# Optimization experiments

Measured on AMD Instinct MI355X. Metric: run time of the kernel, lower is better.

## Reference

```python
import jax, jax.numpy as jnp
import numpy as np

B, S, D_IN, D_OUT, H = 4, 2048, 1024, 1024, 16
D_HEAD = D_OUT // H


def setup_inputs() -> dict:
    key = jax.random.key(0)
    ks = jax.random.split(key, 6)
    sc = 0.02
    return {
        "x": jax.random.normal(ks[0], (B, S, D_IN), dtype=jnp.float32),
        "Wq": jax.random.normal(ks[1], (D_IN, D_OUT), dtype=jnp.float32) * sc,
        "Wk": jax.random.normal(ks[2], (D_IN, D_OUT), dtype=jnp.float32) * sc,
        "Wv": jax.random.normal(ks[3], (D_IN, D_OUT), dtype=jnp.float32) * sc,
        "Wo": jax.random.normal(ks[4], (D_OUT, D_OUT), dtype=jnp.float32) * sc,
        "bo": jnp.zeros((D_OUT,), dtype=jnp.float32),
    }


def reference(x, Wq, Wk, Wv, Wo, bo):
    n_batch, n_tok, _ = x.shape
    # QKV projections (no bias), reshape to [B, H, S, Dh]
    q = (x @ Wq).reshape(n_batch, n_tok, H, D_HEAD).transpose(0, 2, 1, 3)
    k = (x @ Wk).reshape(n_batch, n_tok, H, D_HEAD).transpose(0, 2, 1, 3)
    v = (x @ Wv).reshape(n_batch, n_tok, H, D_HEAD).transpose(0, 2, 1, 3)
    # scores [B, H, S, S], causal mask, scaled softmax
    scores = jnp.einsum('bhqd,bhkd->bhqk', q, k)
    causal = jnp.tril(jnp.ones((n_tok, n_tok), dtype=bool))
    scores = jnp.where(causal, scores, -jnp.inf)
    attn = jax.nn.softmax(scores / jnp.sqrt(jnp.float32(D_HEAD)), axis=-1)
    # dropout in eval mode -> identity
    ctx = jnp.einsum('bhqk,bhkd->bhqd', attn, v)
    ctx = ctx.transpose(0, 2, 1, 3).reshape(n_batch, n_tok, D_OUT)
    return ctx @ Wo + bo
```

## Files before the change

### kernel.cpp

```cpp
#include <hip/hip_runtime.h>


#define S_LEN 2048
#define DMODEL 1024
#define NB 4

typedef unsigned short u16;
typedef float f32x4 __attribute__((ext_vector_type(4)));
typedef short s16x8 __attribute__((ext_vector_type(8)));
typedef __bf16 bf16x8 __attribute__((ext_vector_type(8)));

__device__ __forceinline__ u16 f2bf(float f) {
  return __builtin_bit_cast(u16, (__bf16)f);
}

__device__ __forceinline__ f32x4 mfma16(s16x8 a, s16x8 b, f32x4 c) {
  return __builtin_amdgcn_mfma_f32_16x16x32_bf16(
      __builtin_bit_cast(bf16x8, a), __builtin_bit_cast(bf16x8, b), c, 0, 0, 0);
}

__device__ __forceinline__ void gload_lds16(void* lds, const void* g) {
  __builtin_amdgcn_global_load_lds(
      (const __attribute__((address_space(1))) void*)g,
      (__attribute__((address_space(3))) void*)lds, 16, 0, 0);
}

__device__ __forceinline__ s16x8 lds_frag(const u16* lds, int row, int colb) {
  int addr = (row << 7) + (colb ^ ((row & 7) << 4));
  return *(const s16x8*)((const char*)lds + addr);
}

struct G8 {
  u16 As[3][256 * 64];
  u16 Bs[3][128 * 64];
};

template <int NT>
__device__ __forceinline__ void gemm8ph(const u16* __restrict__ A,
                                        const u16* __restrict__ Bt,
                                        int m0, int n0, G8& L,
                                        f32x4 (&acc)[4][4], int tid) {
  constexpr int K = NT * 64;
  const int lane = tid & 63;
  const int wr = (tid >> 6) >> 1, wc = (tid >> 6) & 1;

  auto SA = [&](int buf, int kt) {
    const u16* g = A + (size_t)m0 * K + kt * 64;
    #pragma unroll
    for (int it = 0; it < 4; ++it) {
      int o = (tid + it * 512) << 4;
      int r = o >> 7, c = o & 127;
      gload_lds16((char*)L.As[buf] + o,
                  (const char*)(g + (size_t)r * K) + (c ^ ((r & 7) << 4)));
    }
  };
  auto SB = [&](int buf, int kt) {
    const u16* g = Bt + (size_t)n0 * K + kt * 64;
    #pragma unroll
    for (int it = 0; it < 2; ++it) {
      int o = (tid + it * 512) << 4;
      int r = o >> 7, c = o & 127;
      gload_lds16((char*)L.Bs[buf] + o,
                  (const char*)(g + (size_t)r * K) + (c ^ ((r & 7) << 4)));
    }
  };

  SA(0, 0); SB(0, 0);
  SA(1, 1); SB(1, 1);
  asm volatile("s_waitcnt vmcnt(6)" ::: "memory");
  asm volatile("s_barrier" ::: "memory");

  int cb = 0;
  for (int t = 0; t < NT; ++t) {
    const u16* Ac = L.As[cb];
    const u16* Bc = L.Bs[cb];
    int nxt = cb + 2; if (nxt >= 3) nxt -= 3;
    bool pf = (t + 2 < NT);
    #pragma unroll
    for (int ph = 0; ph < 2; ++ph) {
      s16x8 a[4], b[4];
      #pragma unroll
      for (int f = 0; f < 4; ++f) {
        a[f] = lds_frag(Ac, wr * 64 + f * 16 + (lane & 15), ph * 64 + ((lane >> 4) << 4));
        b[f] = lds_frag(Bc, wc * 64 + f * 16 + (lane & 15), ph * 64 + ((lane >> 4) << 4));
      }
      if (pf) { if (ph == 0) SA(nxt, t + 2); else SB(nxt, t + 2); }
      asm volatile("s_barrier" ::: "memory");
      asm volatile("s_waitcnt lgkmcnt(0)" ::: "memory");
      __builtin_amdgcn_sched_barrier(0);
      __builtin_amdgcn_s_setprio(1);
      #pragma unroll
      for (int mf = 0; mf < 4; ++mf)
        #pragma unroll
        for (int nf = 0; nf < 4; ++nf)
          acc[mf][nf] = mfma16(a[mf], b[nf], acc[mf][nf]);
      __builtin_amdgcn_s_setprio(0);
    }
    if (pf) asm volatile("s_waitcnt vmcnt(6)" ::: "memory");
    else    asm volatile("s_waitcnt vmcnt(0)" ::: "memory");
    asm volatile("s_barrier" ::: "memory");
    cb = (cb + 1 == 3) ? 0 : cb + 1;
  }
}

__global__ __launch_bounds__(256) void castx_kernel(const float4* __restrict__ x,
                                                    ushort4* __restrict__ xb) {
  int i = blockIdx.x * 256 + threadIdx.x;
  float4 v = x[i];
  ushort4 o;
  o.x = f2bf(v.x); o.y = f2bf(v.y); o.z = f2bf(v.z); o.w = f2bf(v.w);
  xb[i] = o;
}

__global__ __launch_bounds__(256) void wtrans_kernel(
    const float* __restrict__ W0, const float* __restrict__ W1,
    const float* __restrict__ W2, const float* __restrict__ W3,
    u16* __restrict__ T0, u16* __restrict__ T1, u16* __restrict__ T2, u16* __restrict__ T3) {
  int z = blockIdx.z;
  const float* W = (z == 0) ? W0 : (z == 1) ? W1 : (z == 2) ? W2 : W3;
  u16* T = (z == 0) ? T0 : (z == 1) ? T1 : (z == 2) ? T2 : T3;
  __shared__ float t[32][33];
  int n0 = blockIdx.x << 5, k0 = blockIdx.y << 5;
  int tx = threadIdx.x & 31, ty = threadIdx.x >> 5;
  #pragma unroll
  for (int j = 0; j < 4; ++j)
    t[ty + (j << 3)][tx] = W[(size_t)(k0 + ty + (j << 3)) * DMODEL + n0 + tx];
  __syncthreads();
  #pragma unroll
  for (int j = 0; j < 4; ++j)
    T[(size_t)(n0 + ty + (j << 3)) * DMODEL + k0 + tx] = f2bf(t[tx][ty + (j << 3)]);
}

__global__ __launch_bounds__(512, 2) void qkv8_kernel(
    const u16* __restrict__ xb, const u16* __restrict__ WqkvT,
    u16* __restrict__ Qo, u16* __restrict__ Ko, u16* __restrict__ Vo) {
  __shared__ G8 L;
  int bid = blockIdx.x;
  int f = (bid & 7) * 96 + (bid >> 3);
  int m0 = (f / 24) << 8, n0 = (f % 24) << 7;
  int tid = threadIdx.x, lane = tid & 63;
  int wr = (tid >> 6) >> 1, wc = (tid >> 6) & 1;
  f32x4 acc[4][4] = {};
  gemm8ph<16>(xb, WqkvT, m0, n0, L, acc, tid);
  #pragma unroll
  for (int mf = 0; mf < 4; ++mf)
    #pragma unroll
    for (int nf = 0; nf < 4; ++nf)
      #pragma unroll
      for (int i = 0; i < 4; ++i) {
        int rm = m0 + wr * 64 + mf * 16 + ((lane >> 4) << 2) + i;
        int cn = n0 + wc * 64 + nf * 16 + (lane & 15);
        int bb = rm >> 11, s = rm & (S_LEN - 1);
        int z = cn >> 10, c1 = cn & 1023;
        int h = c1 >> 6, d = c1 & 63;
        u16* out = (z == 0) ? Qo : (z == 1) ? Ko : Vo;
        float v = acc[mf][nf][i] * ((z == 0) ? 0.18033688f : 1.0f);
        out[((size_t)((bb << 4) + h) << 17) + ((size_t)s << 6) + d] = f2bf(v);
      }
}

__global__ __launch_bounds__(256) void vtrans_kernel(const u16* __restrict__ V,
                                                     u16* __restrict__ Vt) {
  __shared__ u16 t[64][72];
  int s0 = blockIdx.x << 6;
  size_t bh = blockIdx.y;
  const u16* Vb = V + (bh << 17);
  u16* Vtb = Vt + (bh << 17);
  int tid = threadIdx.x;
  #pragma unroll
  for (int it = 0; it < 2; ++it) {
    int o = (tid + (it << 8)) << 3;
    int r = o >> 6, c = o & 63;
    const ushort4* p = (const ushort4*)(Vb + (((size_t)(s0 + r)) << 6) + c);
    ushort4 v0 = p[0], v1 = p[1];
    t[r][c + 0] = v0.x; t[r][c + 1] = v0.y; t[r][c + 2] = v0.z; t[r][c + 3] = v0.w;
    t[r][c + 4] = v1.x; t[r][c + 5] = v1.y; t[r][c + 6] = v1.z; t[r][c + 7] = v1.w;
  }
  __syncthreads();
  #pragma unroll
  for (int it = 0; it < 2; ++it) {
    int o = (tid + (it << 8)) << 3;
    int d = o >> 6, sl = o & 63;
    ushort4 a, b;
    a.x = t[sl + 0][d]; a.y = t[sl + 1][d]; a.z = t[sl + 2][d]; a.w = t[sl + 3][d];
    b.x = t[sl + 4][d]; b.y = t[sl + 5][d]; b.z = t[sl + 6][d]; b.w = t[sl + 7][d];
    ushort4* q = (ushort4*)(Vtb + ((size_t)d << 11) + s0 + sl);
    q[0] = a; q[1] = b;
  }
}

__global__ __launch_bounds__(512, 4) void attn_kernel(const u16* __restrict__ Q,
                                                      const u16* __restrict__ K,
                                                      const u16* __restrict__ Vt,
                                                      u16* __restrict__ ctx) {
  __shared__ u16 Ks[2][64 * 64];
  __shared__ u16 Vts[2][64 * 64];
  __shared__ u16 Ps[8][16 * 64];
  int bh = blockIdx.x, pid = blockIdx.y;
  int tid = threadIdx.x, lane = tid & 63, w = tid >> 6;
  const u16* Qb = Q + ((size_t)bh << 17);
  const u16* Kb = K + ((size_t)bh << 17);
  const u16* Vtb = Vt + ((size_t)bh << 17);
  int bb = bh >> 4, h = bh & 15;
  u16* Pw = Ps[w];

  s16x8 onesf;
  #pragma unroll
  for (int j = 0; j < 8; ++j) onesf[j] = (short)0x3F80;

  auto stage = [&](int buf, int k0) {
    int o = tid << 4;
    int r = o >> 7, c = o & 127;
    int csrc = c ^ ((r & 7) << 4);
    gload_lds16((char*)Ks[buf] + o, (const char*)(Kb + ((size_t)(k0 + r) << 6)) + csrc);
    gload_lds16((char*)Vts[buf] + o, (const char*)(Vtb + ((size_t)r << 11) + k0) + csrc);
  };

  for (int ph = 0; ph < 2; ++ph) {
    int qblk = ph ? (15 - pid) : pid;
    int q0 = qblk << 7;
    int qw = q0 + (w << 4);

    s16x8 qf[2];
    #pragma unroll
    for (int ks = 0; ks < 2; ++ks) {
      int row = qw + (lane & 15);
      int col = ks * 32 + ((lane >> 4) << 3);
      qf[ks] = *(const s16x8*)(Qb + ((size_t)row << 6) + col);
    }

    f32x4 acc_o[4] = {};
    f32x4 acc_l = {};

    int ntiles = (q0 >> 6) + 2;
    int cur = 0;
    stage(0, 0);
    __syncthreads();
    for (int t = 0; t < ntiles; ++t) {
      int k0 = t << 6;
      if (t + 1 < ntiles) stage(cur ^ 1, (t + 1) << 6);

      bool active = (k0 <= qw + 15);
      if (active) {
        const u16* Kc = Ks[cur];
        const u16* Vc = Vts[cur];
        f32x4 sc[4] = {};
        #pragma unroll
        for (int ks = 0; ks < 2; ++ks) {
          s16x8 kf[4];
          #pragma unroll
          for (int nf = 0; nf < 4; ++nf)
            kf[nf] = lds_frag(Kc, nf * 16 + (lane & 15), ks * 64 + ((lane >> 4) << 4));
          __builtin_amdgcn_s_setprio(1);
          #pragma unroll
          for (int nf = 0; nf < 4; ++nf)
            sc[nf] = mfma16(qf[ks], kf[nf], sc[nf]);
          __builtin_amdgcn_s_setprio(0);
        }

        bool need_mask = (k0 + 63) > qw;
        if (need_mask) {
          #pragma unroll
          for (int i = 0; i < 4; ++i) {
            int q = qw + ((lane >> 4) << 2) + i;
            #pragma unroll
            for (int nf = 0; nf < 4; ++nf) {
              int kv = k0 + nf * 16 + (lane & 15);
              sc[nf][i] = (kv <= q) ? sc[nf][i] : -3.0e38f;
            }
          }
        }
        #pragma unroll
        for (int nf = 0; nf < 4; ++nf)
          #pragma unroll
          for (int i = 0; i < 4; ++i)
            sc[nf][i] = __builtin_amdgcn_exp2f(sc[nf][i]);

        #pragma unroll
        for (int nf = 0; nf < 4; ++nf)
          #pragma unroll
          for (int i = 0; i < 4; ++i) {
            int r = ((lane >> 4) << 2) + i;
            int cb = (nf * 16 + (lane & 15)) << 1;
            *(u16*)((char*)Pw + (r << 7) + (cb ^ ((r & 7) << 4))) = f2bf(sc[nf][i]);
          }
        asm volatile("s_waitcnt lgkmcnt(0)" ::: "memory");
        __builtin_amdgcn_sched_barrier(0);

        #pragma unroll
        for (int ks = 0; ks < 2; ++ks) {
          s16x8 pf = lds_frag(Pw, lane & 15, ks * 64 + ((lane >> 4) << 4));
          s16x8 vf[4];
          #pragma unroll
          for (int nf = 0; nf < 4; ++nf)
            vf[nf] = lds_frag(Vc, nf * 16 + (lane & 15), ks * 64 + ((lane >> 4) << 4));
          __builtin_amdgcn_s_setprio(1);
          #pragma unroll
          for (int nf = 0; nf < 4; ++nf)
            acc_o[nf] = mfma16(pf, vf[nf], acc_o[nf]);
          acc_l = mfma16(pf, onesf, acc_l);
          __builtin_amdgcn_s_setprio(0);
        }
      }
      __syncthreads();
      cur ^= 1;
    }

    #pragma unroll
    for (int i = 0; i < 4; ++i) acc_l[i] = 1.0f / acc_l[i];
    #pragma unroll
    for (int nf = 0; nf < 4; ++nf)
      #pragma unroll
      for (int i = 0; i < 4; ++i) {
        int q = qw + ((lane >> 4) << 2) + i;
        int d = nf * 16 + (lane & 15);
        float v = acc_o[nf][i] * acc_l[i];
        ctx[(((size_t)(bb << 11) + q) << 10) + (h << 6) + d] = f2bf(v);
      }
  }
}

__global__ __launch_bounds__(512, 2) void out8_kernel(const u16* __restrict__ ctx,
                                                      const u16* __restrict__ WoT,
                                                      const float* __restrict__ bo,
                                                      float* __restrict__ out) {
  __shared__ G8 L;
  int bid = blockIdx.x;
  int f = (bid & 7) * 32 + (bid >> 3);
  int m0 = (f >> 3) << 8, n0 = (f & 7) << 7;
  int tid = threadIdx.x, lane = tid & 63;
  int wr = (tid >> 6) >> 1, wc = (tid >> 6) & 1;
  f32x4 acc[4][4] = {};
  gemm8ph<16>(ctx, WoT, m0, n0, L, acc, tid);
  #pragma unroll
  for (int mf = 0; mf < 4; ++mf)
    #pragma unroll
    for (int nf = 0; nf < 4; ++nf)
      #pragma unroll
      for (int i = 0; i < 4; ++i) {
        int rm = m0 + wr * 64 + mf * 16 + ((lane >> 4) << 2) + i;
        int cn = n0 + wc * 64 + nf * 16 + (lane & 15);
        out[(size_t)rm * DMODEL + cn] = acc[mf][nf][i] + bo[cn];
      }
}

extern "C" void kernel_launch(void* const* d_in, const int* in_sizes, int n_in,
                              void* d_out, int out_size, void* d_ws, size_t ws_size,
                              hipStream_t stream) {
  const float* x  = (const float*)d_in[0];
  const float* Wq = (const float*)d_in[1];
  const float* Wk = (const float*)d_in[2];
  const float* Wv = (const float*)d_in[3];
  const float* Wo = (const float*)d_in[4];
  const float* bo = (const float*)d_in[5];
  float* out = (float*)d_out;

  char* ws = (char*)d_ws;
  const size_t SZ_T = (size_t)NB * S_LEN * DMODEL * 2;
  const size_t SZ_W = (size_t)DMODEL * DMODEL * 2;
  u16* xb  = (u16*)(ws);
  u16* WqT = (u16*)(ws + SZ_T);
  u16* WkT = (u16*)(ws + SZ_T + 1 * SZ_W);
  u16* WvT = (u16*)(ws + SZ_T + 2 * SZ_W);
  u16* WoT = (u16*)(ws + SZ_T + 3 * SZ_W);
  u16* Qb  = (u16*)(ws + 1 * SZ_T + 4 * SZ_W);
  u16* Kb  = (u16*)(ws + 2 * SZ_T + 4 * SZ_W);
  u16* Vb  = (u16*)(ws + 3 * SZ_T + 4 * SZ_W);
  u16* Vtb = (u16*)(ws + 4 * SZ_T + 4 * SZ_W);
  u16* ctx = xb;

  castx_kernel<<<dim3((NB * S_LEN * DMODEL / 4) / 256), dim3(256), 0, stream>>>(
      (const float4*)x, (ushort4*)xb);
  wtrans_kernel<<<dim3(32, 32, 4), dim3(256), 0, stream>>>(Wq, Wk, Wv, Wo,
                                                           WqT, WkT, WvT, WoT);
  qkv8_kernel<<<dim3(768), dim3(512), 0, stream>>>(xb, WqT, Qb, Kb, Vb);
  vtrans_kernel<<<dim3(32, 64), dim3(256), 0, stream>>>(Vb, Vtb);
  attn_kernel<<<dim3(64, 8), dim3(512), 0, stream>>>(Qb, Kb, Vtb, ctx);
  out8_kernel<<<dim3(256), dim3(512), 0, stream>>>(ctx, WoT, bo, out);
}
```

Measured before the change: 160.0 us.

## Restructure attention to 32x32 MFMA with transposed scores and register-resident P

The attention kernel moves from 16x16x32 to 32x32x16 MFMA tiles and computes S transposed (K·Q), so each lane owns one query row. P is converted to bf16 in registers and rearranged with v_permlane32_swap instead of going through LDS. Each warp now covers 32 query rows, with 4 warps per block instead of 8. The row sum becomes a per-lane scalar accumulation instead of an MFMA against a ones vector. This removes the LDS round trip, its waitcnt barrier and the extra MFMA for l, but raises register pressure and halves the threads per block.

```diff
diff --git a/kernel.cpp b/kernel.cpp
--- a/kernel.cpp
+++ b/kernel.cpp
@@ -6,7 +6,10 @@
 #define NB 4
 
 typedef unsigned short u16;
+typedef unsigned int u32;
 typedef float f32x4 __attribute__((ext_vector_type(4)));
+typedef float f32x16 __attribute__((ext_vector_type(16)));
+typedef int i32x4 __attribute__((ext_vector_type(4)));
 typedef short s16x8 __attribute__((ext_vector_type(8)));
 typedef __bf16 bf16x8 __attribute__((ext_vector_type(8)));
 
@@ -17,6 +20,17 @@
 __device__ __forceinline__ f32x4 mfma16(s16x8 a, s16x8 b, f32x4 c) {
   return __builtin_amdgcn_mfma_f32_16x16x32_bf16(
       __builtin_bit_cast(bf16x8, a), __builtin_bit_cast(bf16x8, b), c, 0, 0, 0);
+}
+
+__device__ __forceinline__ f32x16 mfma32(s16x8 a, s16x8 b, f32x16 c) {
+  return __builtin_amdgcn_mfma_f32_32x32x16_bf16(
+      __builtin_bit_cast(bf16x8, a), __builtin_bit_cast(bf16x8, b), c, 0, 0, 0);
+}
+
+__device__ __forceinline__ int cvtpk(float a, float b) {
+  int r;
+  asm("v_cvt_pk_bf16_f32 %0, %1, %2" : "=v"(r) : "v"(a), "v"(b));
+  return r;
 }
 
 __device__ __forceinline__ void gload_lds16(void* lds, const void* g) {
@@ -189,48 +203,44 @@
   }
 }
 
-__global__ __launch_bounds__(512, 4) void attn_kernel(const u16* __restrict__ Q,
+__global__ __launch_bounds__(256, 2) void attn_kernel(const u16* __restrict__ Q,
                                                       const u16* __restrict__ K,
                                                       const u16* __restrict__ Vt,
                                                       u16* __restrict__ ctx) {
   __shared__ u16 Ks[2][64 * 64];
   __shared__ u16 Vts[2][64 * 64];
-  __shared__ u16 Ps[8][16 * 64];
   int bh = blockIdx.x, pid = blockIdx.y;
   int tid = threadIdx.x, lane = tid & 63, w = tid >> 6;
+  int hi = lane >> 5, lq = lane & 31;
   const u16* Qb = Q + ((size_t)bh << 17);
   const u16* Kb = K + ((size_t)bh << 17);
   const u16* Vtb = Vt + ((size_t)bh << 17);
   int bb = bh >> 4, h = bh & 15;
-  u16* Pw = Ps[w];
-
-  s16x8 onesf;
-  #pragma unroll
-  for (int j = 0; j < 8; ++j) onesf[j] = (short)0x3F80;
 
   auto stage = [&](int buf, int k0) {
-    int o = tid << 4;
-    int r = o >> 7, c = o & 127;
-    int csrc = c ^ ((r & 7) << 4);
-    gload_lds16((char*)Ks[buf] + o, (const char*)(Kb + ((size_t)(k0 + r) << 6)) + csrc);
-    gload_lds16((char*)Vts[buf] + o, (const char*)(Vtb + ((size_t)r << 11) + k0) + csrc);
+    #pragma unroll
+    for (int it = 0; it < 2; ++it) {
+      int o = (tid + (it << 8)) << 4;
+      int r = o >> 7, c = o & 127;
+      int csrc = c ^ ((r & 7) << 4);
+      gload_lds16((char*)Ks[buf] + o, (const char*)(Kb + ((size_t)(k0 + r) << 6)) + csrc);
+      gload_lds16((char*)Vts[buf] + o, (const char*)(Vtb + ((size_t)r << 11) + k0) + csrc);
+    }
   };
 
   for (int ph = 0; ph < 2; ++ph) {
     int qblk = ph ? (15 - pid) : pid;
     int q0 = qblk << 7;
-    int qw = q0 + (w << 4);
-
-    s16x8 qf[2];
-    #pragma unroll
-    for (int ks = 0; ks < 2; ++ks) {
-      int row = qw + (lane & 15);
-      int col = ks * 32 + ((lane >> 4) << 3);
-      qf[ks] = *(const s16x8*)(Qb + ((size_t)row << 6) + col);
-    }
-
-    f32x4 acc_o[4] = {};
-    f32x4 acc_l = {};
+    int qw = q0 + (w << 5);
+    int q = qw + lq;
+
+    s16x8 qf[4];
+    #pragma unroll
+    for (int t = 0; t < 4; ++t)
+      qf[t] = *(const s16x8*)(Qb + ((size_t)q << 6) + t * 16 + (hi << 3));
+
+    f32x16 acc_o[2] = {};
+    float l_acc = 0.0f;
 
     int ntiles = (q0 >> 6) + 2;
     int cur = 0;
@@ -239,83 +249,66 @@
     for (int t = 0; t < ntiles; ++t) {
       int k0 = t << 6;
       if (t + 1 < ntiles) stage(cur ^ 1, (t + 1) << 6);
-
-      bool active = (k0 <= qw + 15);
-      if (active) {
-        const u16* Kc = Ks[cur];
-        const u16* Vc = Vts[cur];
-        f32x4 sc[4] = {};
-        #pragma unroll
-        for (int ks = 0; ks < 2; ++ks) {
-          s16x8 kf[4];
+      const u16* Kc = Ks[cur];
+      const u16* Vc = Vts[cur];
+
+      #pragma unroll
+      for (int kvb = 0; kvb < 2; ++kvb) {
+        int kb0 = k0 + kvb * 32;
+        if (kb0 <= qw + 31) {
+          f32x16 sc = {};
           #pragma unroll
-          for (int nf = 0; nf < 4; ++nf)
-            kf[nf] = lds_frag(Kc, nf * 16 + (lane & 15), ks * 64 + ((lane >> 4) << 4));
-          __builtin_amdgcn_s_setprio(1);
-          #pragma unroll
-          for (int nf = 0; nf < 4; ++nf)
-            sc[nf] = mfma16(qf[ks], kf[nf], sc[nf]);
-          __builtin_amdgcn_s_setprio(0);
-        }
-
-        bool need_mask = (k0 + 63) > qw;
-        if (need_mask) {
-          #pragma unroll
-          for (int i = 0; i < 4; ++i) {
-            int q = qw + ((lane >> 4) << 2) + i;
+          for (int tt = 0; tt < 4; ++tt) {
+            s16x8 kf = lds_frag(Kc, kvb * 32 + lq, tt * 32 + (hi << 4));
+            sc = mfma32(kf, qf[tt], sc);
+          }
+          if (kb0 + 31 > qw) {
             #pragma unroll
-            for (int nf = 0; nf < 4; ++nf) {
-              int kv = k0 + nf * 16 + (lane & 15);
-              sc[nf][i] = (kv <= q) ? sc[nf][i] : -3.0e38f;
+            for (int r = 0; r < 16; ++r) {
+              int kv = kb0 + (r & 3) + ((r >> 2) << 3) + (hi << 2);
+              sc[r] = (kv <= q) ? sc[r] : -3.0e38f;
             }
           }
-        }
-        #pragma unroll
-        for (int nf = 0; nf < 4; ++nf)
           #pragma unroll
-          for (int i = 0; i < 4; ++i)
-            sc[nf][i] = __builtin_amdgcn_exp2f(sc[nf][i]);
-
-        #pragma unroll
-        for (int nf = 0; nf < 4; ++nf)
+          for (int r = 0; r < 16; ++r) sc[r] = __builtin_amdgcn_exp2f(sc[r]);
           #pragma unroll
-          for (int i = 0; i < 4; ++i) {
-            int r = ((lane >> 4) << 2) + i;
-            int cb = (nf * 16 + (lane & 15)) << 1;
-            *(u16*)((char*)Pw + (r << 7) + (cb ^ ((r & 7) << 4))) = f2bf(sc[nf][i]);
+          for (int r = 0; r < 16; ++r) l_acc += sc[r];
+
+          #pragma unroll
+          for (int tt = 0; tt < 2; ++tt) {
+            int x0 = cvtpk(sc[8 * tt + 0], sc[8 * tt + 1]);
+            int x1 = cvtpk(sc[8 * tt + 2], sc[8 * tt + 3]);
+            int y0 = cvtpk(sc[8 * tt + 4], sc[8 * tt + 5]);
+            int y1 = cvtpk(sc[8 * tt + 6], sc[8 * tt + 7]);
+            asm volatile("v_permlane32_swap_b32 %0, %1" : "+v"(x0), "+v"(y0));
+            asm volatile("v_permlane32_swap_b32 %0, %1" : "+v"(x1), "+v"(y1));
+            i32x4 wi = {x0, x1, y0, y1};
+            s16x8 W = __builtin_bit_cast(s16x8, wi);
+            int tg = kvb * 2 + tt;
+            __builtin_amdgcn_s_setprio(1);
+            #pragma unroll
+            for (int dblk = 0; dblk < 2; ++dblk) {
+              s16x8 vf = lds_frag(Vc, dblk * 32 + lq, tg * 32 + (hi << 4));
+              acc_o[dblk] = mfma32(vf, W, acc_o[dblk]);
+            }
+            __builtin_amdgcn_s_setprio(0);
           }
-        asm volatile("s_waitcnt lgkmcnt(0)" ::: "memory");
-        __builtin_amdgcn_sched_barrier(0);
-
-        #pragma unroll
-        for (int ks = 0; ks < 2; ++ks) {
-          s16x8 pf = lds_frag(Pw, lane & 15, ks * 64 + ((lane >> 4) << 4));
-          s16x8 vf[4];
-          #pragma unroll
-          for (int nf = 0; nf < 4; ++nf)
-            vf[nf] = lds_frag(Vc, nf * 16 + (lane & 15), ks * 64 + ((lane >> 4) << 4));
-          __builtin_amdgcn_s_setprio(1);
-          #pragma unroll
-          for (int nf = 0; nf < 4; ++nf)
-            acc_o[nf] = mfma16(pf, vf[nf], acc_o[nf]);
-          acc_l = mfma16(pf, onesf, acc_l);
-          __builtin_amdgcn_s_setprio(0);
         }
       }
       __syncthreads();
       cur ^= 1;
     }
 
-    #pragma unroll
-    for (int i = 0; i < 4; ++i) acc_l[i] = 1.0f / acc_l[i];
-    #pragma unroll
-    for (int nf = 0; nf < 4; ++nf)
-      #pragma unroll
-      for (int i = 0; i < 4; ++i) {
-        int q = qw + ((lane >> 4) << 2) + i;
-        int d = nf * 16 + (lane & 15);
-        float v = acc_o[nf][i] * acc_l[i];
-        ctx[(((size_t)(bb << 11) + q) << 10) + (h << 6) + d] = f2bf(v);
+    l_acc += __shfl_xor(l_acc, 32);
+    float linv = 1.0f / l_acc;
+    #pragma unroll
+    for (int dblk = 0; dblk < 2; ++dblk)
+      #pragma unroll
+      for (int rp = 0; rp < 8; ++rp) {
+        int r = rp * 2;
+        int pk = cvtpk(acc_o[dblk][r] * linv, acc_o[dblk][r + 1] * linv);
+        int d = dblk * 32 + (r & 3) + ((r >> 2) << 3) + (hi << 2);
+        *(u32*)(ctx + (((size_t)(bb << 11) + q) << 10) + (h << 6) + d) = (u32)pk;
       }
   }
 }
@@ -375,6 +368,6 @@
                                                            WqT, WkT, WvT, WoT);
   qkv8_kernel<<<dim3(768), dim3(512), 0, stream>>>(xb, WqT, Qb, Kb, Vb);
   vtrans_kernel<<<dim3(32, 64), dim3(256), 0, stream>>>(Vb, Vtb);
-  attn_kernel<<<dim3(64, 8), dim3(512), 0, stream>>>(Qb, Kb, Vtb, ctx);
+  attn_kernel<<<dim3(64, 8), dim3(256), 0, stream>>>(Qb, Kb, Vtb, ctx);
   out8_kernel<<<dim3(256), dim3(512), 0, stream>>>(ctx, WoT, bo, out);
 }
```

New measurement: 154.0 us. -3.8%, faster.
